# Optimization experiments

Measured on AMD Instinct MI355X. Metric: run time of the kernel, lower is better.

The kernel has to match this reference:

```python
import jax, jax.numpy as jnp
import numpy as np

D_MODEL = 1024
N_HEADS = 16
B, T = 2, 2048


def setup_inputs() -> dict:
    key = jax.random.key(0)
    kx, kqkv, ko = jax.random.split(key, 3)
    x = jax.random.normal(kx, (B, T, D_MODEL), dtype=jnp.float32)
    # flax Linear default init (lecun_normal ~ scaled); plain scaled normal is fine for a baseline
    Wqkv = jax.random.normal(kqkv, (D_MODEL, 3 * D_MODEL), dtype=jnp.float32) / np.sqrt(D_MODEL)
    Wo = jax.random.normal(ko, (D_MODEL, D_MODEL), dtype=jnp.float32) / np.sqrt(D_MODEL)
    return {"x": x, "Wqkv": Wqkv, "Wo": Wo}


def reference(x, Wqkv, Wo):
    Bx, Tx, C = x.shape
    H = N_HEADS
    Hd = C // H
    scale = C ** (-0.5)  # NOTE: module scales by d_model**-0.5, not head_dim**-0.5
    qkv = x @ Wqkv  # [B, T, 3C]
    q, k, v = jnp.split(qkv, 3, axis=-1)
    q = q.reshape(Bx, Tx, H, Hd).transpose(0, 2, 1, 3)  # [B,H,T,Hd]
    k = k.reshape(Bx, Tx, H, Hd).transpose(0, 2, 1, 3)
    v = v.reshape(Bx, Tx, H, Hd).transpose(0, 2, 1, 3)
    attn = jnp.einsum('bhid,bhjd->bhij', q, k) * scale  # [B,H,T,T]
    mask = jnp.tril(jnp.ones((Tx, Tx), dtype=jnp.bool_))
    attn = jnp.where(mask[None, None], attn, jnp.finfo(attn.dtype).min)
    attn = jax.nn.softmax(attn.astype(jnp.float32), axis=-1).astype(attn.dtype)
    out = jnp.einsum('bhij,bhjd->bhid', attn, v)  # [B,H,T,Hd]
    out = out.transpose(0, 2, 1, 3).reshape(Bx, Tx, C)
    return out @ Wo
```

## Files before the change

### kernel.cpp

```cpp
#include <hip/hip_runtime.h>
#include <cstdint>
#include <math.h>

#define D_MODEL 1024
#define N_HEADS 16
#define HEAD_DIM 64
#define BB 2
#define TT 2048
#define QSCALE 0.04508422002778011f
#define MSTATIC 12.0f

typedef float f32x4 __attribute__((ext_vector_type(4)));
typedef __bf16 bf16x8 __attribute__((ext_vector_type(8)));

__device__ inline ushort f2bf(float f) {
    union { float f; uint32_t u; } c; c.f = f;
    uint32_t u = c.u;
    uint32_t r = (u + 0x7FFFu + ((u >> 16) & 1u)) >> 16;
    return (ushort)r;
}
__device__ inline ushort f2bf_hw(float f) {
    __bf16 h = (__bf16)f;
    return __builtin_bit_cast(ushort, h);
}

__device__ inline void load_lds16(const ushort* g, ushort* lds_uniform_base) {
    __builtin_amdgcn_global_load_lds(
        (const __attribute__((address_space(1))) uint32_t*)g,
        (__attribute__((address_space(3))) uint32_t*)lds_uniform_base, 16, 0, 0);
}

__global__ __launch_bounds__(256) void conv_x(
    const float4* __restrict__ in, ushort4* __restrict__ out, int n4)
{
    int i = blockIdx.x * 256 + threadIdx.x;
    if (i < n4) {
        float4 v = in[i];
        ushort4 u;
        u.x = f2bf(v.x); u.y = f2bf(v.y); u.z = f2bf(v.z); u.w = f2bf(v.w);
        out[i] = u;
    }
}

__global__ __launch_bounds__(256) void transpose_f32_bf16(
    const float* __restrict__ in, ushort* __restrict__ out, int R, int C)
{
    __shared__ ushort tile[32][33];
    int tx = threadIdx.x;
    int ty = threadIdx.y;
    int c0 = blockIdx.x * 32;
    int r0 = blockIdx.y * 32;
#pragma unroll
    for (int i = 0; i < 32; i += 8)
        tile[ty + i][tx] = f2bf(in[(size_t)(r0 + ty + i) * C + (c0 + tx)]);
    __syncthreads();
#pragma unroll
    for (int i = 0; i < 32; i += 8)
        out[(size_t)(c0 + ty + i) * R + (r0 + tx)] = tile[tx][ty + i];
}

__device__ inline void gemm128_mainloop(
    const ushort* __restrict__ A, const ushort* __restrict__ BT,
    int rowBase, int colBase, ushort* Al, ushort* Bl,
    f32x4 acc[4][4], int wave, int lane)
{
    const int K = D_MODEL;
    int lr = lane & 15, quad = lane >> 4;
    int lrow = lane >> 2;
    int kq = lane & 3;
    int mq = (wave >> 1) * 64, nq = (wave & 1) * 64;

    const ushort* gA0 = A + (size_t)(rowBase + wave * 32 + lrow) * K + kq * 8;
    const ushort* gA1 = gA0 + (size_t)16 * K;
    const ushort* gB0 = BT + (size_t)(colBase + wave * 32 + lrow) * K + kq * 8;
    const ushort* gB1 = gB0 + (size_t)16 * K;
    ushort* lA0 = Al + (wave * 32) * 32;
    ushort* lA1 = Al + (wave * 32 + 16) * 32;
    ushort* lB0 = Bl + (wave * 32) * 32;
    ushort* lB1 = Bl + (wave * 32 + 16) * 32;

    for (int kt = 0; kt < K / 32; ++kt) {
        __syncthreads();
        int ko = kt * 32;
        load_lds16(gA0 + ko, lA0);
        load_lds16(gA1 + ko, lA1);
        load_lds16(gB0 + ko, lB0);
        load_lds16(gB1 + ko, lB1);
        __syncthreads();
        bf16x8 af[4], bf[4];
#pragma unroll
        for (int mi = 0; mi < 4; ++mi)
            af[mi] = *(const bf16x8*)(Al + (mq + mi * 16 + lr) * 32 + quad * 8);
#pragma unroll
        for (int ni = 0; ni < 4; ++ni)
            bf[ni] = *(const bf16x8*)(Bl + (nq + ni * 16 + lr) * 32 + quad * 8);
#pragma unroll
        for (int mi = 0; mi < 4; ++mi)
#pragma unroll
            for (int ni = 0; ni < 4; ++ni)
                acc[mi][ni] = __builtin_amdgcn_mfma_f32_16x16x32_bf16(
                    af[mi], bf[ni], acc[mi][ni], 0, 0, 0);
    }
}

__global__ __launch_bounds__(256) void gemm_qkv(
    const ushort* __restrict__ A, const ushort* __restrict__ BT,
    ushort* __restrict__ Qo, ushort* __restrict__ Ko, ushort* __restrict__ VTo)
{
    __shared__ ushort Al[128 * 32];
    __shared__ ushort Bl[128 * 32];
    int tid = threadIdx.x;
    int wave = tid >> 6, lane = tid & 63;
    int lr = lane & 15, quad = lane >> 4;
    int rowBase = blockIdx.y * 128;
    int colBase = blockIdx.x * 128;
    f32x4 acc[4][4] = {};
    gemm128_mainloop(A, BT, rowBase, colBase, Al, Bl, acc, wave, lane);

    int mq = (wave >> 1) * 64, nq = (wave & 1) * 64;
#pragma unroll
    for (int ni = 0; ni < 4; ++ni) {
        int n = colBase + nq + ni * 16 + lr;
        int s = n >> 10;
        int cc = n & 1023;
        int h = cc >> 6, d = cc & 63;
        float scale = (s == 0) ? QSCALE : 1.0f;
#pragma unroll
        for (int mi = 0; mi < 4; ++mi) {
#pragma unroll
            for (int i = 0; i < 4; ++i) {
                int m = rowBase + mq + mi * 16 + quad * 4 + i;
                int b = m >> 11, t = m & 2047;
                int bh = b * N_HEADS + h;
                if (s == 2) {
                    VTo[((size_t)bh * HEAD_DIM + d) * TT + t] = f2bf(acc[mi][ni][i]);
                } else {
                    ushort* dst = (s == 0) ? Qo : Ko;
                    dst[((size_t)bh * TT + t) * HEAD_DIM + d] = f2bf(acc[mi][ni][i] * scale);
                }
            }
        }
    }
}

__global__ __launch_bounds__(256) void gemm_plain(
    const ushort* __restrict__ A, const ushort* __restrict__ BT,
    float* __restrict__ O, int N)
{
    __shared__ ushort Al[128 * 32];
    __shared__ ushort Bl[128 * 32];
    int tid = threadIdx.x;
    int wave = tid >> 6, lane = tid & 63;
    int lr = lane & 15, quad = lane >> 4;
    int rowBase = blockIdx.y * 128;
    int colBase = blockIdx.x * 128;
    f32x4 acc[4][4] = {};
    gemm128_mainloop(A, BT, rowBase, colBase, Al, Bl, acc, wave, lane);

    int mq = (wave >> 1) * 64, nq = (wave & 1) * 64;
#pragma unroll
    for (int mi = 0; mi < 4; ++mi)
#pragma unroll
        for (int ni = 0; ni < 4; ++ni) {
            int n = colBase + nq + ni * 16 + lr;
#pragma unroll
            for (int i = 0; i < 4; ++i) {
                int m = rowBase + mq + mi * 16 + quad * 4 + i;
                O[(size_t)m * N + n] = acc[mi][ni][i];
            }
        }
}

__global__ __launch_bounds__(256) void attn_flash(
    const ushort* __restrict__ Q,
    const ushort* __restrict__ K,
    const ushort* __restrict__ VT,
    ushort* __restrict__ AO)
{
    int bid = blockIdx.x;
    int bh  = bid & 31;
    int idx = bid >> 5;
    int qi  = (idx < 8) ? idx : (23 - idx);
    int tid = threadIdx.x;
    int wave = tid >> 6, lane = tid & 63;
    int quad = lane >> 4, lr = lane & 15;
    int qw = qi * 128 + wave * 32;

    const ushort* Qb = Q  + (size_t)bh * TT * HEAD_DIM;
    const ushort* Kb = K  + (size_t)bh * TT * HEAD_DIM;
    const ushort* Vb = VT + (size_t)bh * HEAD_DIM * TT;

    __shared__ ushort pbuf[4][32][40];
    ushort (*P)[40] = pbuf[wave];

    bf16x8 qa[2][2];
#pragma unroll
    for (int r = 0; r < 2; ++r)
#pragma unroll
        for (int s = 0; s < 2; ++s)
            qa[r][s] = *(const bf16x8*)(Qb + (size_t)(qw + r * 16 + lr) * HEAD_DIM
                                           + s * 32 + quad * 8);

    f32x4 o[2][4] = {};
    f32x4 l[2] = {};

    bf16x8 ones;
#pragma unroll
    for (int j = 0; j < 8; ++j) ones[j] = (__bf16)1.0f;

    int ktiles = (qw >> 5) + 1;
    for (int kt = 0; kt < ktiles; ++kt) {
        int k0 = kt << 5;
        bf16x8 kb[2][2];
#pragma unroll
        for (int c = 0; c < 2; ++c)
#pragma unroll
            for (int s = 0; s < 2; ++s)
                kb[c][s] = *(const bf16x8*)(Kb + (size_t)(k0 + c * 16 + lr) * HEAD_DIM
                                               + s * 32 + quad * 8);
        f32x4 sc[2][2];
#pragma unroll
        for (int r = 0; r < 2; ++r)
#pragma unroll
            for (int c = 0; c < 2; ++c)
#pragma unroll
                for (int i = 0; i < 4; ++i) sc[r][c][i] = -MSTATIC;
#pragma unroll
        for (int r = 0; r < 2; ++r)
#pragma unroll
            for (int c = 0; c < 2; ++c) {
                sc[r][c] = __builtin_amdgcn_mfma_f32_16x16x32_bf16(qa[r][0], kb[c][0], sc[r][c], 0, 0, 0);
                sc[r][c] = __builtin_amdgcn_mfma_f32_16x16x32_bf16(qa[r][1], kb[c][1], sc[r][c], 0, 0, 0);
            }
        if (kt == ktiles - 1) {
#pragma unroll
            for (int r = 0; r < 2; ++r)
#pragma unroll
                for (int c = 0; c < 2; ++c)
#pragma unroll
                    for (int i = 0; i < 4; ++i)
                        if (c * 16 + lr > r * 16 + quad * 4 + i) sc[r][c][i] = -3e38f;
        }
        bf16x8 vb[4];
#pragma unroll
        for (int d = 0; d < 4; ++d)
            vb[d] = *(const bf16x8*)(Vb + (size_t)(d * 16 + lr) * TT + k0 + quad * 8);

#pragma unroll
        for (int r = 0; r < 2; ++r)
#pragma unroll
            for (int c = 0; c < 2; ++c)
#pragma unroll
                for (int i = 0; i < 4; ++i)
                    P[r * 16 + quad * 4 + i][c * 16 + lr] =
                        f2bf_hw(__builtin_amdgcn_exp2f(sc[r][c][i]));

#pragma unroll
        for (int r = 0; r < 2; ++r) {
            bf16x8 pa = *(const bf16x8*)&P[r * 16 + lr][quad * 8];
            l[r] = __builtin_amdgcn_mfma_f32_16x16x32_bf16(pa, ones, l[r], 0, 0, 0);
#pragma unroll
            for (int d = 0; d < 4; ++d)
                o[r][d] = __builtin_amdgcn_mfma_f32_16x16x32_bf16(pa, vb[d], o[r][d], 0, 0, 0);
        }
    }

    int b = bh >> 4, h = bh & 15;
#pragma unroll
    for (int r = 0; r < 2; ++r) {
        f32x4 rl;
#pragma unroll
        for (int i = 0; i < 4; ++i) rl[i] = 1.0f / l[r][i];
#pragma unroll
        for (int d = 0; d < 4; ++d)
#pragma unroll
            for (int i = 0; i < 4; ++i) {
                int row = qw + r * 16 + quad * 4 + i;
                AO[((size_t)(b * TT + row)) * D_MODEL + h * HEAD_DIM + d * 16 + lr] =
                    f2bf(o[r][d][i] * rl[i]);
            }
    }
}

extern "C" void kernel_launch(void* const* d_in, const int* in_sizes, int n_in,
                              void* d_out, int out_size, void* d_ws, size_t ws_size,
                              hipStream_t stream)
{
    (void)in_sizes; (void)n_in; (void)out_size; (void)ws_size;
    const float* x    = (const float*)d_in[0];
    const float* Wqkv = (const float*)d_in[1];
    const float* Wo   = (const float*)d_in[2];
    float* out = (float*)d_out;

    char* ws = (char*)d_ws;
    size_t off = 0;
    ushort* WqkvT = (ushort*)(ws + off); off += (size_t)3 * D_MODEL * D_MODEL * 2;
    ushort* WoT   = (ushort*)(ws + off); off += (size_t)D_MODEL * D_MODEL * 2;
    ushort* xb    = (ushort*)(ws + off); off += (size_t)BB * TT * D_MODEL * 2;
    ushort* Qd    = (ushort*)(ws + off); off += (size_t)BB * D_MODEL * TT * 2;
    ushort* Kd    = (ushort*)(ws + off); off += (size_t)BB * D_MODEL * TT * 2;
    ushort* VTd   = (ushort*)(ws + off); off += (size_t)BB * D_MODEL * TT * 2;
    ushort* AO    = (ushort*)(ws + off); off += (size_t)BB * TT * D_MODEL * 2;

    int n4 = BB * TT * D_MODEL / 4;
    conv_x<<<dim3(n4 / 256), 256, 0, stream>>>(
        (const float4*)x, (ushort4*)xb, n4);

    transpose_f32_bf16<<<dim3(3 * D_MODEL / 32, D_MODEL / 32), dim3(32, 8), 0, stream>>>(
        Wqkv, WqkvT, D_MODEL, 3 * D_MODEL);
    transpose_f32_bf16<<<dim3(D_MODEL / 32, D_MODEL / 32), dim3(32, 8), 0, stream>>>(
        Wo, WoT, D_MODEL, D_MODEL);

    gemm_qkv<<<dim3(3 * D_MODEL / 128, BB * TT / 128), 256, 0, stream>>>(
        xb, WqkvT, Qd, Kd, VTd);

    attn_flash<<<dim3(512), 256, 0, stream>>>(Qd, Kd, VTd, AO);

    gemm_plain<<<dim3(D_MODEL / 128, BB * TT / 128), 256, 0, stream>>>(
        AO, WoT, out, D_MODEL);
}
```

Baseline: 238.3 us.

## Split attention KV loop across two wave halves and combine via LDS

Doubles the attention block to 512 threads. The two groups of four waves process alternating key tiles for the same query rows, and the partial output and row-sum accumulators are then merged through shared memory before normalization and the store. Because softmax uses a static max, the partials can simply be added. This halves the serial key-loop length per wave to increase parallelism on the attention kernel, which has only 512 blocks. The cost is a larger shared-memory footprint, a block-wide barrier with a combine step, and a larger register budget per block that could lower occupancy.

Result: no change. 235.9 us (-1.0%).

```diff
diff --git a/kernel.cpp b/kernel.cpp
--- a/kernel.cpp
+++ b/kernel.cpp
@@ -171,7 +171,7 @@
         }
 }
 
-__global__ __launch_bounds__(256) void attn_flash(
+__global__ __launch_bounds__(512) void attn_flash(
     const ushort* __restrict__ Q,
     const ushort* __restrict__ K,
     const ushort* __restrict__ VT,
@@ -182,15 +182,19 @@
     int idx = bid >> 5;
     int qi  = (idx < 8) ? idx : (23 - idx);
     int tid = threadIdx.x;
-    int wave = tid >> 6, lane = tid & 63;
+    int wave = tid >> 6;
+    int pair = wave & 3;
+    int half = wave >> 2;
+    int lane = tid & 63;
     int quad = lane >> 4, lr = lane & 15;
-    int qw = qi * 128 + wave * 32;
+    int qw = qi * 128 + pair * 32;
 
     const ushort* Qb = Q  + (size_t)bh * TT * HEAD_DIM;
     const ushort* Kb = K  + (size_t)bh * TT * HEAD_DIM;
     const ushort* Vb = VT + (size_t)bh * HEAD_DIM * TT;
 
-    __shared__ ushort pbuf[4][32][40];
+    __shared__ ushort pbuf[8][32][40];
+    __shared__ float comb[4][10][64][4];
     ushort (*P)[40] = pbuf[wave];
 
     bf16x8 qa[2][2];
@@ -209,7 +213,7 @@
     for (int j = 0; j < 8; ++j) ones[j] = (__bf16)1.0f;
 
     int ktiles = (qw >> 5) + 1;
-    for (int kt = 0; kt < ktiles; ++kt) {
+    for (int kt = half; kt < ktiles; kt += 2) {
         int k0 = kt << 5;
         bf16x8 kb[2][2];
 #pragma unroll
@@ -265,20 +269,42 @@
         }
     }
 
-    int b = bh >> 4, h = bh & 15;
-#pragma unroll
-    for (int r = 0; r < 2; ++r) {
-        f32x4 rl;
-#pragma unroll
-        for (int i = 0; i < 4; ++i) rl[i] = 1.0f / l[r][i];
-#pragma unroll
-        for (int d = 0; d < 4; ++d)
-#pragma unroll
-            for (int i = 0; i < 4; ++i) {
-                int row = qw + r * 16 + quad * 4 + i;
-                AO[((size_t)(b * TT + row)) * D_MODEL + h * HEAD_DIM + d * 16 + lr] =
-                    f2bf(o[r][d][i] * rl[i]);
-            }
+    if (half == 1) {
+#pragma unroll
+        for (int r = 0; r < 2; ++r)
+#pragma unroll
+            for (int d = 0; d < 4; ++d)
+                *(f32x4*)&comb[pair][r * 4 + d][lane][0] = o[r][d];
+#pragma unroll
+        for (int r = 0; r < 2; ++r)
+            *(f32x4*)&comb[pair][8 + r][lane][0] = l[r];
+    }
+    __syncthreads();
+    if (half == 0) {
+#pragma unroll
+        for (int r = 0; r < 2; ++r)
+#pragma unroll
+            for (int d = 0; d < 4; ++d)
+                o[r][d] += *(const f32x4*)&comb[pair][r * 4 + d][lane][0];
+#pragma unroll
+        for (int r = 0; r < 2; ++r)
+            l[r] += *(const f32x4*)&comb[pair][8 + r][lane][0];
+
+        int b = bh >> 4, h = bh & 15;
+#pragma unroll
+        for (int r = 0; r < 2; ++r) {
+            f32x4 rl;
+#pragma unroll
+            for (int i = 0; i < 4; ++i) rl[i] = 1.0f / l[r][i];
+#pragma unroll
+            for (int d = 0; d < 4; ++d)
+#pragma unroll
+                for (int i = 0; i < 4; ++i) {
+                    int row = qw + r * 16 + quad * 4 + i;
+                    AO[((size_t)(b * TT + row)) * D_MODEL + h * HEAD_DIM + d * 16 + lr] =
+                        f2bf(o[r][d][i] * rl[i]);
+                }
+        }
     }
 }
 
@@ -314,7 +340,7 @@
     gemm_qkv<<<dim3(3 * D_MODEL / 128, BB * TT / 128), 256, 0, stream>>>(
         xb, WqkvT, Qd, Kd, VTd);
 
-    attn_flash<<<dim3(512), 256, 0, stream>>>(Qd, Kd, VTd, AO);
+    attn_flash<<<dim3(512), 512, 0, stream>>>(Qd, Kd, VTd, AO);
 
     gemm_plain<<<dim3(D_MODEL / 128, BB * TT / 128), 256, 0, stream>>>(
         AO, WoT, out, D_MODEL);
```
